# Kernel optimization log

Hardware: AMD Instinct MI355X
Metric: run time of the kernel (lower is better)

Reference implementation:

```python
import jax, jax.numpy as jnp
import numpy as np

NINF = -1000000000.0
B, S, E = 2, 4096, 1024


def setup_inputs() -> dict:
    key = jax.random.key(0)
    ks = jax.random.split(key, 10)
    scale = 1.0 / np.sqrt(E)
    return {
        "query": jax.random.normal(ks[0], (B, S, E), dtype=jnp.float32),
        "key": jax.random.normal(ks[1], (B, S, E), dtype=jnp.float32),
        "value": jax.random.normal(ks[2], (B, S, E), dtype=jnp.float32),
        "mask": jax.random.randint(ks[3], (S, S), 0, 2).astype(bool),
        "Wq": jax.random.normal(ks[4], (E, E), dtype=jnp.float32) * scale,
        "bq": jnp.zeros((E,), dtype=jnp.float32),
        "Wk": jax.random.normal(ks[5], (E, E), dtype=jnp.float32) * scale,
        "bk": jnp.zeros((E,), dtype=jnp.float32),
        "Wv": jax.random.normal(ks[6], (E, E), dtype=jnp.float32) * scale,
        "bv": jnp.zeros((E,), dtype=jnp.float32),
    }


def reference(query, key, value, mask, Wq, bq, Wk, bk, Wv, bv):
    # linear projections (nn.Linear convention: x @ W.T + b)
    q = jnp.einsum('bse,fe->bsf', query, Wq) + bq   # [B,S,E]
    k = jnp.einsum('bse,fe->bsf', key, Wk) + bk
    v = jnp.einsum('bse,fe->bsf', value, Wv) + bv
    # full QK^T score matrix [B,S,S], scaled by sqrt(E) of projected query
    scores = jnp.einsum('bqe,bke->bqk', q, k) / jnp.sqrt(jnp.float32(E))
    scores = jnp.where(mask, jnp.float32(NINF), scores)  # True = ignored
    attn = jax.nn.softmax(scores, axis=-1)
    return jnp.einsum('bqk,bkv->bqv', attn, v)
```

## Files before the change

### kernel.cpp

```cpp
#include <hip/hip_runtime.h>
#include <hip/hip_bf16.h>


typedef _Float16 f16_t;
typedef _Float16 f16x8 __attribute__((ext_vector_type(8)));
typedef float f32x4 __attribute__((ext_vector_type(4)));
typedef unsigned long long u64;

union PackH8 { f16x8 v; f16_t e[8]; };

__device__ __forceinline__ f32x4 mfma_f16(f16x8 a, f16x8 b, f32x4 c) {
  return __builtin_amdgcn_mfma_f32_16x16x32_f16(a, b, c, 0, 0, 0);
}

__device__ __forceinline__ void cp16(const f16_t* g, f16_t* l) {
  __builtin_amdgcn_global_load_lds(
      (const __attribute__((address_space(1))) unsigned int*)g,
      (__attribute__((address_space(3))) unsigned int*)l, 16, 0, 0);
}

__global__ __launch_bounds__(256) void cvt_mask(
    const float* __restrict__ q, const float* __restrict__ k,
    const float* __restrict__ v, const float* __restrict__ wq,
    const float* __restrict__ wk, const float* __restrict__ wv,
    const int* __restrict__ mask,
    f16_t* __restrict__ xq, f16_t* __restrict__ xk, f16_t* __restrict__ xv,
    f16_t* __restrict__ wqh, f16_t* __restrict__ wkh, f16_t* __restrict__ wvh,
    u64* __restrict__ mb) {
  if (blockIdx.y == 6) {
    const int lane = threadIdx.x & 63;
    int wid = blockIdx.x * 4 + (threadIdx.x >> 6);
    for (int w = wid; w < 262144; w += 16384) {
      const int pred = mask[(size_t)w * 64 + lane] != 0;
      u64 b = __ballot(pred);
      if (lane == 0) mb[w] = b;
    }
    return;
  }
  const float* src; f16_t* dst; size_t n;
  switch (blockIdx.y) {
    case 0: src = q;  dst = xq;  n = 8388608; break;
    case 1: src = k;  dst = xk;  n = 8388608; break;
    case 2: src = v;  dst = xv;  n = 8388608; break;
    case 3: src = wq; dst = wqh; n = 1048576; break;
    case 4: src = wk; dst = wkh; n = 1048576; break;
    default: src = wv; dst = wvh; n = 1048576; break;
  }
  size_t i = ((size_t)blockIdx.x * 256 + threadIdx.x) * 8;
  if (i >= n) return;
  float4 a = *(const float4*)(src + i);
  float4 b = *(const float4*)(src + i + 4);
  PackH8 p;
  p.e[0] = (f16_t)a.x; p.e[1] = (f16_t)a.y; p.e[2] = (f16_t)a.z; p.e[3] = (f16_t)a.w;
  p.e[4] = (f16_t)b.x; p.e[5] = (f16_t)b.y; p.e[6] = (f16_t)b.z; p.e[7] = (f16_t)b.w;
  *(f16x8*)(dst + i) = p.v;
}

#define TK 64

__global__ __launch_bounds__(512, 2) void gemm512(
    const f16_t* __restrict__ A, const f16_t* __restrict__ B,
    f16_t* __restrict__ C, const float* __restrict__ bias0,
    const float* __restrict__ bias1, int K,
    long sAz, long sBz, long sCz, float scale0, float scale1, int Cstride) {
  __shared__ f16_t sA[256 * TK];
  __shared__ f16_t sB[256 * TK];

  const int bz = blockIdx.z;
  const int n0 = blockIdx.x * 256;
  const int m0 = blockIdx.y * 256;
  const int tid = threadIdx.x;
  const int w = tid >> 6, lane = tid & 63;
  const int quad = lane >> 4, l15 = lane & 15;
  const int wm = w >> 1, wn = w & 1;
  const int lr = lane >> 3, ls = lane & 7;
  const int sw = ls ^ lr;

  const f16_t* Ab = A + (size_t)sAz * bz;
  const f16_t* Bb = B + (size_t)sBz * bz;

  const f16_t* ga[4];
  const f16_t* gb[4];
#pragma unroll
  for (int j = 0; j < 4; j++) {
    ga[j] = Ab + (size_t)(m0 + w * 32 + j * 8 + lr) * K + sw * 8;
    gb[j] = Bb + (size_t)(n0 + w * 32 + j * 8 + lr) * K + sw * 8;
  }

  f32x4 acc[4][8] = {};

  for (int k0 = 0; k0 < K; k0 += TK) {
    __syncthreads();
#pragma unroll
    for (int j = 0; j < 4; j++) {
      cp16(ga[j] + k0, &sA[(w * 32 + j * 8) * TK]);
      cp16(gb[j] + k0, &sB[(w * 32 + j * 8) * TK]);
    }
    __syncthreads();
#pragma unroll
    for (int ks = 0; ks < 2; ks++) {
      f16x8 af[4], bf[8];
#pragma unroll
      for (int mi = 0; mi < 4; mi++) {
        const int row = wm * 64 + mi * 16 + l15;
        const int sg = (ks * 4 + quad) ^ (row & 7);
        af[mi] = *(const f16x8*)&sA[row * TK + sg * 8];
      }
#pragma unroll
      for (int ni = 0; ni < 8; ni++) {
        const int row = wn * 128 + ni * 16 + l15;
        const int sg = (ks * 4 + quad) ^ (row & 7);
        bf[ni] = *(const f16x8*)&sB[row * TK + sg * 8];
      }
#pragma unroll
      for (int mi = 0; mi < 4; mi++)
#pragma unroll
        for (int ni = 0; ni < 8; ni++)
          acc[mi][ni] = mfma_f16(af[mi], bf[ni], acc[mi][ni]);
    }
  }

  const float* bias = bz ? bias1 : bias0;
  const float scale = bz ? scale1 : scale0;
  f16_t* Cb = C + (size_t)sCz * bz;
#pragma unroll
  for (int mi = 0; mi < 4; mi++) {
#pragma unroll
    for (int ni = 0; ni < 8; ni++) {
      const int gm0 = m0 + wm * 64 + mi * 16 + quad * 4;
      const int gn = n0 + wn * 128 + ni * 16 + l15;
#pragma unroll
      for (int r = 0; r < 4; r++) {
        const int gm = gm0 + r;
        Cb[(size_t)gm * Cstride + gn] = (f16_t)((acc[mi][ni][r] + bias[gn]) * scale);
      }
    }
  }
}

__global__ __launch_bounds__(256, 2) void gemm256(
    const f16_t* __restrict__ A, const f16_t* __restrict__ B,
    f16_t* __restrict__ C, const float* __restrict__ bias0, int K) {
  __shared__ f16_t sA[256 * TK];
  __shared__ f16_t sB[128 * TK];

  const int n0 = blockIdx.x * 128;
  const int m0 = blockIdx.y * 256;
  const int tid = threadIdx.x;
  const int w = tid >> 6, lane = tid & 63;
  const int quad = lane >> 4, l15 = lane & 15;
  const int lr = lane >> 3, ls = lane & 7;
  const int sw = ls ^ lr;

  const f16_t* ga[8];
  const f16_t* gb[4];
#pragma unroll
  for (int j = 0; j < 8; j++)
    ga[j] = A + (size_t)(m0 + w * 64 + j * 8 + lr) * K + sw * 8;
#pragma unroll
  for (int j = 0; j < 4; j++)
    gb[j] = B + (size_t)(n0 + w * 32 + j * 8 + lr) * K + sw * 8;

  f32x4 acc[4][8] = {};

  for (int k0 = 0; k0 < K; k0 += TK) {
    __syncthreads();
#pragma unroll
    for (int j = 0; j < 8; j++) cp16(ga[j] + k0, &sA[(w * 64 + j * 8) * TK]);
#pragma unroll
    for (int j = 0; j < 4; j++) cp16(gb[j] + k0, &sB[(w * 32 + j * 8) * TK]);
    __syncthreads();
#pragma unroll
    for (int ks = 0; ks < 2; ks++) {
      f16x8 af[4], bf[8];
#pragma unroll
      for (int mi = 0; mi < 4; mi++) {
        const int row = w * 64 + mi * 16 + l15;
        const int sg = (ks * 4 + quad) ^ (row & 7);
        af[mi] = *(const f16x8*)&sA[row * TK + sg * 8];
      }
#pragma unroll
      for (int ni = 0; ni < 8; ni++) {
        const int row = ni * 16 + l15;
        const int sg = (ks * 4 + quad) ^ (row & 7);
        bf[ni] = *(const f16x8*)&sB[row * TK + sg * 8];
      }
#pragma unroll
      for (int mi = 0; mi < 4; mi++)
#pragma unroll
        for (int ni = 0; ni < 8; ni++)
          acc[mi][ni] = mfma_f16(af[mi], bf[ni], acc[mi][ni]);
    }
  }

#pragma unroll
  for (int mi = 0; mi < 4; mi++) {
#pragma unroll
    for (int ni = 0; ni < 8; ni++) {
      const int gm0 = m0 + w * 64 + mi * 16 + quad * 4;
      const int gn = n0 + ni * 16 + l15;
#pragma unroll
      for (int r = 0; r < 4; r++) {
        const int gm = gm0 + r;
        const int bb = gn >> 12;
        const int s = gn & 4095;
        C[(size_t)bb * 4194304 + (size_t)gm * 4096 + s] =
            (f16_t)(acc[mi][ni][r] + bias0[gm]);
      }
    }
  }
}

__global__ __launch_bounds__(512, 2) void gemm_qk(
    const f16_t* __restrict__ A, const f16_t* __restrict__ B,
    f16_t* __restrict__ S, const u64* __restrict__ mb,
    float* __restrict__ lrow) {
  __shared__ f16_t sA[256 * TK];
  __shared__ f16_t sB[256 * TK];

  const int bz = blockIdx.z;
  const int n0 = blockIdx.x * 256;
  const int m0 = blockIdx.y * 256;
  const int tid = threadIdx.x;
  const int w = tid >> 6, lane = tid & 63;
  const int quad = lane >> 4, l15 = lane & 15;
  const int wm = w >> 1, wn = w & 1;
  const int lr = lane >> 3, ls = lane & 7;
  const int sw = ls ^ lr;

  const f16_t* Ab = A + (size_t)4194304 * bz;
  const f16_t* Bb = B + (size_t)4194304 * bz;

  const f16_t* ga[4];
  const f16_t* gb[4];
#pragma unroll
  for (int j = 0; j < 4; j++) {
    ga[j] = Ab + (size_t)(m0 + w * 32 + j * 8 + lr) * 1024 + sw * 8;
    gb[j] = Bb + (size_t)(n0 + w * 32 + j * 8 + lr) * 1024 + sw * 8;
  }

  f32x4 acc[4][8] = {};

  for (int k0 = 0; k0 < 1024; k0 += TK) {
    __syncthreads();
#pragma unroll
    for (int j = 0; j < 4; j++) {
      cp16(ga[j] + k0, &sA[(w * 32 + j * 8) * TK]);
      cp16(gb[j] + k0, &sB[(w * 32 + j * 8) * TK]);
    }
    __syncthreads();
#pragma unroll
    for (int ks = 0; ks < 2; ks++) {
      f16x8 af[4], bf[8];
#pragma unroll
      for (int mi = 0; mi < 4; mi++) {
        const int row = wm * 64 + mi * 16 + l15;
        const int sg = (ks * 4 + quad) ^ (row & 7);
        af[mi] = *(const f16x8*)&sA[row * TK + sg * 8];
      }
#pragma unroll
      for (int ni = 0; ni < 8; ni++) {
        const int row = wn * 128 + ni * 16 + l15;
        const int sg = (ks * 4 + quad) ^ (row & 7);
        bf[ni] = *(const f16x8*)&sB[row * TK + sg * 8];
      }
#pragma unroll
      for (int mi = 0; mi < 4; mi++)
#pragma unroll
        for (int ni = 0; ni < 8; ni++)
          acc[mi][ni] = mfma_f16(af[mi], bf[ni], acc[mi][ni]);
    }
  }

  f16_t* Sb = S + (size_t)16777216 * bz;
  float* lb = lrow + bz * 4096;
  const int wbase = (n0 >> 6) + wn * 2;
#pragma unroll
  for (int mi = 0; mi < 4; mi++) {
#pragma unroll
    for (int r = 0; r < 4; r++) {
      const int gm = m0 + wm * 64 + mi * 16 + quad * 4 + r;
      const u64 w0 = mb[(size_t)gm * 64 + wbase];
      const u64 w1 = mb[(size_t)gm * 64 + wbase + 1];
      float rs = 0.f;
#pragma unroll
      for (int ni = 0; ni < 8; ni++) {
        const int col_l = ni * 16 + l15;
        const u64 mw = (ni < 4) ? w0 : w1;
        const int bit = (int)((mw >> (col_l & 63)) & 1);
        const float p = bit ? 0.f : __expf(acc[mi][ni][r] - 3.0f);
        Sb[(size_t)gm * 4096 + n0 + wn * 128 + col_l] = (f16_t)p;
        rs += p;
      }
      rs += __shfl_xor(rs, 1); rs += __shfl_xor(rs, 2);
      rs += __shfl_xor(rs, 4); rs += __shfl_xor(rs, 8);
      if (l15 == 0) atomicAdd(&lb[gm], rs);
    }
  }
}

__global__ __launch_bounds__(256) void gemm_pv(
    const f16_t* __restrict__ S, const f16_t* __restrict__ V,
    float* __restrict__ O, const float* __restrict__ lrow) {
  __shared__ f16_t sA[128 * TK];
  __shared__ f16_t sB[128 * TK];
  const int bid = blockIdx.x;
  const int bz = bid >> 8;
  const int r8 = bid & 255;
  const int xcd = r8 & 7;
  const int j = r8 >> 3;
  const int m0 = (xcd * 4 + (j >> 3)) * 128;
  const int n0 = (j & 7) * 128;

  const int tid = threadIdx.x;
  const int w = tid >> 6, lane = tid & 63;
  const int quad = lane >> 4, l15 = lane & 15;
  const int wm = w >> 1, wn = w & 1;
  const int lr = lane >> 3, ls = lane & 7;
  const int sw = ls ^ lr;

  const f16_t* Ab = S + (size_t)16777216 * bz;
  const f16_t* Bb = V + (size_t)4194304 * bz;

  const f16_t* ga[4];
  const f16_t* gb[4];
#pragma unroll
  for (int jj = 0; jj < 4; jj++) {
    ga[jj] = Ab + (size_t)(m0 + w * 32 + jj * 8 + lr) * 4096 + sw * 8;
    gb[jj] = Bb + (size_t)(n0 + w * 32 + jj * 8 + lr) * 4096 + sw * 8;
  }

  f32x4 acc[4][4] = {};

  for (int k0 = 0; k0 < 4096; k0 += TK) {
    __syncthreads();
#pragma unroll
    for (int jj = 0; jj < 4; jj++) {
      cp16(ga[jj] + k0, &sA[(w * 32 + jj * 8) * TK]);
      cp16(gb[jj] + k0, &sB[(w * 32 + jj * 8) * TK]);
    }
    __syncthreads();
#pragma unroll
    for (int ks = 0; ks < 2; ks++) {
      f16x8 af[4], bf[4];
#pragma unroll
      for (int mi = 0; mi < 4; mi++) {
        const int row = wm * 64 + mi * 16 + l15;
        const int sg = (ks * 4 + quad) ^ (row & 7);
        af[mi] = *(const f16x8*)&sA[row * TK + sg * 8];
      }
#pragma unroll
      for (int ni = 0; ni < 4; ni++) {
        const int row = wn * 64 + ni * 16 + l15;
        const int sg = (ks * 4 + quad) ^ (row & 7);
        bf[ni] = *(const f16x8*)&sB[row * TK + sg * 8];
      }
#pragma unroll
      for (int mi = 0; mi < 4; mi++)
#pragma unroll
        for (int ni = 0; ni < 4; ni++)
          acc[mi][ni] = mfma_f16(af[mi], bf[ni], acc[mi][ni]);
    }
  }

  float* Ob = O + (size_t)4194304 * bz;
  const float* lb = lrow + bz * 4096;
#pragma unroll
  for (int mi = 0; mi < 4; mi++) {
#pragma unroll
    for (int ni = 0; ni < 4; ni++) {
      const int gm0 = m0 + wm * 64 + mi * 16 + quad * 4;
      const int gn = n0 + wn * 64 + ni * 16 + l15;
#pragma unroll
      for (int r = 0; r < 4; r++) {
        const int gm = gm0 + r;
        Ob[(size_t)gm * 1024 + gn] = acc[mi][ni][r] * (1.0f / lb[gm]);
      }
    }
  }
}

extern "C" void kernel_launch(void* const* d_in, const int* in_sizes, int n_in,
                              void* d_out, int out_size, void* d_ws, size_t ws_size,
                              hipStream_t stream) {
  const float* query = (const float*)d_in[0];
  const float* key_  = (const float*)d_in[1];
  const float* value = (const float*)d_in[2];
  const int* mask    = (const int*)d_in[3];
  const float* Wq = (const float*)d_in[4];
  const float* bq = (const float*)d_in[5];
  const float* Wk = (const float*)d_in[6];
  const float* bk = (const float*)d_in[7];
  const float* Wv = (const float*)d_in[8];
  const float* bv = (const float*)d_in[9];
  float* out = (float*)d_out;

  const size_t MB = (size_t)1 << 20;
  char* w = (char*)d_ws;
  f16_t* qb  = (f16_t*)(w);
  f16_t* kb  = (f16_t*)(w + 16 * MB);
  f16_t* vt  = (f16_t*)(w + 32 * MB);
  f16_t* xq  = (f16_t*)(w + 48 * MB);
  f16_t* xk  = (f16_t*)(w + 64 * MB);
  f16_t* xv  = (f16_t*)(w + 80 * MB);
  f16_t* wqh = (f16_t*)(w + 96 * MB);
  f16_t* wkh = (f16_t*)(w + 98 * MB);
  f16_t* wvh = (f16_t*)(w + 100 * MB);
  f16_t* S   = (f16_t*)(w + 48 * MB);
  float* ls  = (float*)(w + 112 * MB);
  u64* mb = (u64*)d_out;

  cvt_mask<<<dim3(4096, 7), 256, 0, stream>>>(query, key_, value, Wq, Wk, Wv,
                                              mask, xq, xk, xv, wqh, wkh, wvh, mb);
  gemm512<<<dim3(4, 32, 2), 512, 0, stream>>>(
      xq, wqh, qb, bq, bk, 1024, 8388608L, 1048576L, 8388608L,
      0.03125f, 1.0f, 1024);
  gemm256<<<dim3(64, 4), 256, 0, stream>>>(wvh, xv, vt, bv, 1024);
  hipMemsetAsync(ls, 0, 2 * 4096 * sizeof(float), stream);
  gemm_qk<<<dim3(16, 16, 2), 512, 0, stream>>>(qb, kb, S, mb, ls);
  gemm_pv<<<dim3(512), 256, 0, stream>>>(S, vt, out, ls);
}
```

Measured before the change: 434.2 us.

## Replace synchronous GEMM mainloop with 4-stage pipelined 8-phase shared core

Introduces a shared core8ph routine that keeps four 32-wide K slices of A and B in LDS and issues global-to-LDS async copies several phases ahead, waiting with explicit vmcnt counts instead of a full sync per K step. Each phase interleaves half of the fragment loads and MFMAs with one staged copy and uses setprio and sched_barrier to keep the matrix work grouped. The projection and QK^T GEMMs both use it, aiming to hide global load latency behind MFMA work. It uses 128KB of LDS per block, which may limit occupancy to one block per CU, and the wraparound K indexing issues redundant prefetches past the end of K.

Measured after the change: 433.5 us. About the same (-0.2%).

```diff
diff --git a/kernel.cpp b/kernel.cpp
--- a/kernel.cpp
+++ b/kernel.cpp
@@ -6,6 +6,7 @@
 typedef _Float16 f16x8 __attribute__((ext_vector_type(8)));
 typedef float f32x4 __attribute__((ext_vector_type(4)));
 typedef unsigned long long u64;
+typedef unsigned int uint;
 
 union PackH8 { f16x8 v; f16_t e[8]; };
 
@@ -58,68 +59,118 @@
 
 #define TK 64
 
+__device__ __forceinline__ void core8ph(
+    const f16_t* __restrict__ Ab, const f16_t* __restrict__ Bb,
+    int m0, int n0, int K, int iters, f32x4 (&acc)[4][8]) {
+  __shared__ f16_t lA[32768];
+  __shared__ f16_t lB[32768];
+
+  const int tid = threadIdx.x;
+  const int w = tid >> 6, lane = tid & 63;
+  const int quad = lane >> 4, l15 = lane & 15;
+  const int wm = w >> 1, wn = w & 1;
+  const int srow = lane >> 2;
+  const int sg = (lane & 3) ^ (srow & 3);
+  const int Km = K - 1;
+
+  const uint aoff0 = (uint)(m0 + w * 32 + srow) * K + sg * 8;
+  const uint aoff1 = aoff0 + 16 * K;
+  const uint boff0 = (uint)(n0 + w * 32 + srow) * K + sg * 8;
+  const uint boff1 = boff0 + 16 * K;
+  const int ld0 = (w * 32) * 32;
+  const int ld1 = (w * 32 + 16) * 32;
+
+  int afo[4], bfo[8];
+  const int swz = (quad ^ (l15 & 3)) * 8;
+#pragma unroll
+  for (int mi = 0; mi < 4; mi++) afo[mi] = (wm * 64 + mi * 16 + l15) * 32 + swz;
+#pragma unroll
+  for (int ni = 0; ni < 8; ni++) bfo[ni] = (wn * 128 + ni * 16 + l15) * 32 + swz;
+
+#define STG_A(sl, kb) { cp16(Ab + aoff0 + (kb), lA + (sl) * 8192 + ld0); \
+                        cp16(Ab + aoff1 + (kb), lA + (sl) * 8192 + ld1); }
+#define STG_B(sl, kb) { cp16(Bb + boff0 + (kb), lB + (sl) * 8192 + ld0); \
+                        cp16(Bb + boff1 + (kb), lB + (sl) * 8192 + ld1); }
+
+  STG_A(0, 0) STG_B(0, 0)
+  STG_A(1, 32) STG_B(1, 32)
+  STG_A(2, 64) STG_B(2, 64)
+  asm volatile("s_waitcnt vmcnt(4)" ::: "memory");
+  __builtin_amdgcn_s_barrier();
+
+  f16x8 af[4], bf[8];
+
+#define PH(SL, Q, STG, VMW) { \
+    if ((Q) == 0) { \
+      _Pragma("unroll") for (int mi = 0; mi < 4; mi++) \
+        af[mi] = *(const f16x8*)(lA + (SL) * 8192 + afo[mi]); \
+      _Pragma("unroll") for (int ni = 0; ni < 4; ni++) \
+        bf[ni] = *(const f16x8*)(lB + (SL) * 8192 + bfo[ni]); \
+    } else { \
+      _Pragma("unroll") for (int ni = 4; ni < 8; ni++) \
+        bf[ni] = *(const f16x8*)(lB + (SL) * 8192 + bfo[ni]); \
+    } \
+    STG \
+    asm volatile("" ::: "memory"); \
+    __builtin_amdgcn_s_barrier(); \
+    asm volatile("s_waitcnt lgkmcnt(0)" ::: "memory"); \
+    __builtin_amdgcn_sched_barrier(0); \
+    __builtin_amdgcn_s_setprio(1); \
+    _Pragma("unroll") for (int mi = 0; mi < 4; mi++) { \
+      _Pragma("unroll") for (int nj = 0; nj < 4; nj++) { \
+        const int ni = (Q) * 4 + nj; \
+        acc[mi][ni] = mfma_f16(af[mi], bf[ni], acc[mi][ni]); \
+      } } \
+    __builtin_amdgcn_sched_barrier(0); \
+    __builtin_amdgcn_s_setprio(0); \
+    VMW \
+    asm volatile("" ::: "memory"); \
+    __builtin_amdgcn_s_barrier(); \
+  }
+
+#define VM4 asm volatile("s_waitcnt vmcnt(4)" ::: "memory");
+
+  for (int i = 0; i < iters; i++) {
+    const int t0 = 2 * i;
+    const int kb3 = ((t0 + 1) * 64 + 32) & Km;
+    const int kb0 = ((t0 + 2) * 64) & Km;
+    const int kb1 = kb0 + 32;
+    const int kb2 = ((t0 + 3) * 64) & Km;
+    PH(0, 0, STG_A(3, kb3), )
+    PH(0, 1, STG_B(3, kb3), )
+    PH(1, 0, STG_A(0, kb0), )
+    PH(1, 1, STG_B(0, kb0), VM4)
+    PH(2, 0, STG_A(1, kb1), )
+    PH(2, 1, STG_B(1, kb1), )
+    PH(3, 0, STG_A(2, kb2), )
+    PH(3, 1, STG_B(2, kb2), VM4)
+  }
+
+  asm volatile("s_waitcnt vmcnt(0)" ::: "memory");
+#undef PH
+#undef VM4
+#undef STG_A
+#undef STG_B
+}
+
 __global__ __launch_bounds__(512, 2) void gemm512(
     const f16_t* __restrict__ A, const f16_t* __restrict__ B,
     f16_t* __restrict__ C, const float* __restrict__ bias0,
     const float* __restrict__ bias1, int K,
     long sAz, long sBz, long sCz, float scale0, float scale1, int Cstride) {
-  __shared__ f16_t sA[256 * TK];
-  __shared__ f16_t sB[256 * TK];
-
   const int bz = blockIdx.z;
   const int n0 = blockIdx.x * 256;
   const int m0 = blockIdx.y * 256;
+  const f16_t* Ab = A + (size_t)sAz * bz;
+  const f16_t* Bb = B + (size_t)sBz * bz;
+
+  f32x4 acc[4][8] = {};
+  core8ph(Ab, Bb, m0, n0, K, K >> 7, acc);
+
   const int tid = threadIdx.x;
   const int w = tid >> 6, lane = tid & 63;
   const int quad = lane >> 4, l15 = lane & 15;
   const int wm = w >> 1, wn = w & 1;
-  const int lr = lane >> 3, ls = lane & 7;
-  const int sw = ls ^ lr;
-
-  const f16_t* Ab = A + (size_t)sAz * bz;
-  const f16_t* Bb = B + (size_t)sBz * bz;
-
-  const f16_t* ga[4];
-  const f16_t* gb[4];
-#pragma unroll
-  for (int j = 0; j < 4; j++) {
-    ga[j] = Ab + (size_t)(m0 + w * 32 + j * 8 + lr) * K + sw * 8;
-    gb[j] = Bb + (size_t)(n0 + w * 32 + j * 8 + lr) * K + sw * 8;
-  }
-
-  f32x4 acc[4][8] = {};
-
-  for (int k0 = 0; k0 < K; k0 += TK) {
-    __syncthreads();
-#pragma unroll
-    for (int j = 0; j < 4; j++) {
-      cp16(ga[j] + k0, &sA[(w * 32 + j * 8) * TK]);
-      cp16(gb[j] + k0, &sB[(w * 32 + j * 8) * TK]);
-    }
-    __syncthreads();
-#pragma unroll
-    for (int ks = 0; ks < 2; ks++) {
-      f16x8 af[4], bf[8];
-#pragma unroll
-      for (int mi = 0; mi < 4; mi++) {
-        const int row = wm * 64 + mi * 16 + l15;
-        const int sg = (ks * 4 + quad) ^ (row & 7);
-        af[mi] = *(const f16x8*)&sA[row * TK + sg * 8];
-      }
-#pragma unroll
-      for (int ni = 0; ni < 8; ni++) {
-        const int row = wn * 128 + ni * 16 + l15;
-        const int sg = (ks * 4 + quad) ^ (row & 7);
-        bf[ni] = *(const f16x8*)&sB[row * TK + sg * 8];
-      }
-#pragma unroll
-      for (int mi = 0; mi < 4; mi++)
-#pragma unroll
-        for (int ni = 0; ni < 8; ni++)
-          acc[mi][ni] = mfma_f16(af[mi], bf[ni], acc[mi][ni]);
-    }
-  }
-
   const float* bias = bz ? bias1 : bias0;
   const float scale = bz ? scale1 : scale0;
   f16_t* Cb = C + (size_t)sCz * bz;
@@ -215,63 +266,19 @@
     const f16_t* __restrict__ A, const f16_t* __restrict__ B,
     f16_t* __restrict__ S, const u64* __restrict__ mb,
     float* __restrict__ lrow) {
-  __shared__ f16_t sA[256 * TK];
-  __shared__ f16_t sB[256 * TK];
-
   const int bz = blockIdx.z;
   const int n0 = blockIdx.x * 256;
   const int m0 = blockIdx.y * 256;
+  const f16_t* Ab = A + (size_t)4194304 * bz;
+  const f16_t* Bb = B + (size_t)4194304 * bz;
+
+  f32x4 acc[4][8] = {};
+  core8ph(Ab, Bb, m0, n0, 1024, 8, acc);
+
   const int tid = threadIdx.x;
   const int w = tid >> 6, lane = tid & 63;
   const int quad = lane >> 4, l15 = lane & 15;
   const int wm = w >> 1, wn = w & 1;
-  const int lr = lane >> 3, ls = lane & 7;
-  const int sw = ls ^ lr;
-
-  const f16_t* Ab = A + (size_t)4194304 * bz;
-  const f16_t* Bb = B + (size_t)4194304 * bz;
-
-  const f16_t* ga[4];
-  const f16_t* gb[4];
-#pragma unroll
-  for (int j = 0; j < 4; j++) {
-    ga[j] = Ab + (size_t)(m0 + w * 32 + j * 8 + lr) * 1024 + sw * 8;
-    gb[j] = Bb + (size_t)(n0 + w * 32 + j * 8 + lr) * 1024 + sw * 8;
-  }
-
-  f32x4 acc[4][8] = {};
-
-  for (int k0 = 0; k0 < 1024; k0 += TK) {
-    __syncthreads();
-#pragma unroll
-    for (int j = 0; j < 4; j++) {
-      cp16(ga[j] + k0, &sA[(w * 32 + j * 8) * TK]);
-      cp16(gb[j] + k0, &sB[(w * 32 + j * 8) * TK]);
-    }
-    __syncthreads();
-#pragma unroll
-    for (int ks = 0; ks < 2; ks++) {
-      f16x8 af[4], bf[8];
-#pragma unroll
-      for (int mi = 0; mi < 4; mi++) {
-        const int row = wm * 64 + mi * 16 + l15;
-        const int sg = (ks * 4 + quad) ^ (row & 7);
-        af[mi] = *(const f16x8*)&sA[row * TK + sg * 8];
-      }
-#pragma unroll
-      for (int ni = 0; ni < 8; ni++) {
-        const int row = wn * 128 + ni * 16 + l15;
-        const int sg = (ks * 4 + quad) ^ (row & 7);
-        bf[ni] = *(const f16x8*)&sB[row * TK + sg * 8];
-      }
-#pragma unroll
-      for (int mi = 0; mi < 4; mi++)
-#pragma unroll
-        for (int ni = 0; ni < 8; ni++)
-          acc[mi][ni] = mfma_f16(af[mi], bf[ni], acc[mi][ni]);
-    }
-  }
-
   f16_t* Sb = S + (size_t)16777216 * bz;
   float* lb = lrow + bz * 4096;
   const int wbase = (n0 >> 6) + wn * 2;
```
